# Kernel optimization log

Measured on AMD Instinct MI355X. Metric: run time of the kernel, lower is better.

The kernel has to match this reference:

```python
import math
import jax, jax.numpy as jnp
import numpy as np

THETA_BINS = 8
PHI_BINS = 8
BLOCK_SIZE = 15
MAX_PHI = math.pi
DVOL = 64  # input volume is DVOL^3
EPS = 2.220446049250313e-16  # sys.float_info.epsilon


def _sobel_weight():
    # Fixed (3,1,3,3,3) central-difference kernels: channel 0 = d/dz, 1 = d/dy, 2 = d/dx
    w = np.zeros((3, 1, 3, 3, 3), np.float32)
    w[0, 0, 0, 1, 1] = -1.0; w[0, 0, 2, 1, 1] = 1.0  # s_z
    w[1, 0, 1, 0, 1] = -1.0; w[1, 0, 1, 2, 1] = 1.0  # s_y
    w[2, 0, 1, 1, 0] = -1.0; w[2, 0, 1, 1, 2] = 1.0  # s_x
    return jnp.asarray(w)


def setup_inputs() -> dict:
    key = jax.random.key(0)
    x = jax.random.normal(key, (DVOL, DVOL, DVOL), dtype=jnp.float32)
    return {"x": x, "weight": _sobel_weight()}


def reference(x, weight):
    offset = BLOCK_SIZE // 2 + 1  # 8; output spatial = d + 2*offset - 2
    xb = x.astype(jnp.float32)[None, None]  # (1,1,d,h,w)
    out = jax.lax.conv_general_dilated(
        xb, weight, window_strides=(1, 1, 1),
        padding=[(offset, offset)] * 3,
        dimension_numbers=("NCDHW", "OIDHW", "NCDHW"))[0]  # (3, D, H, W)

    mag = jnp.sqrt(jnp.sum(out * out, axis=0))              # (D,H,W) frobenius over channel
    theta = jnp.arctan2(out[1], out[2])
    phi = jnp.arccos(out[0] / (mag + EPS))

    # NOTE: original code divides theta by max_phi_angle and scales by phi_bins (faithful)
    t_raw = theta / MAX_PHI * PHI_BINS
    p_raw = phi / MAX_PHI * PHI_BINS
    t_frac = t_raw - jnp.trunc(t_raw)  # torch.frac semantics
    p_frac = p_raw - jnp.trunc(p_raw)

    i0 = jnp.floor(t_raw).astype(jnp.int32) % THETA_BINS  # theta lower bin
    i1 = jnp.ceil(t_raw).astype(jnp.int32) % THETA_BINS   # theta upper bin
    i2 = jnp.floor(p_raw).astype(jnp.int32) % PHI_BINS    # phi lower bin
    i3 = jnp.ceil(p_raw).astype(jnp.int32) % PHI_BINS     # phi upper bin

    f0 = jnp.abs(t_frac); f1 = jnp.abs(1.0 - t_frac)
    f2 = jnp.abs(p_frac); f3 = jnp.abs(1.0 - p_frac)
    w0 = (f0 * f2) * mag  # scattered to (i0, i2) via scatter_ set
    w1 = (f0 * f3) * mag  # scatter_add at (i0, i3)
    w2 = (f1 * f2) * mag  # scatter_add at (i1, i2)

    # The torch scatter_/scatter_add_ chain (zero fill elsewhere, initial tensor zeros)
    # reduces exactly to three one-hot depositions per voxel; 4th add is absent
    # because the source forward is truncated after the third scatter_add_.
    tb = jnp.arange(THETA_BINS, dtype=jnp.int32)[:, None, None, None]  # (T,1,1,1)
    pb = jnp.arange(PHI_BINS, dtype=jnp.int32)[:, None, None, None]   # (P,1,1,1)
    t0 = (tb == i0).astype(mag.dtype)  # (T,D,H,W)
    t1 = (tb == i1).astype(mag.dtype)
    p2 = (pb == i2).astype(mag.dtype)  # (P,D,H,W)
    p3 = (pb == i3).astype(mag.dtype)

    out_plus_bins = (t0[:, None] * p2[None] * w0
                     + t0[:, None] * p3[None] * w1
                     + t1[:, None] * p2[None] * w2)  # (T,P,D,H,W)
    return out_plus_bins[None]  # (1, theta_bins, phi_bins, D, H, W)
```

## Files before the change

### kernel.cpp

```cpp
#include <hip/hip_runtime.h>
#include <math.h>


#define DVOL 64
#define S 78
#define S3 (S * S * S)
#define S3_4 (S3 / 4)

typedef float f32x4 __attribute__((ext_vector_type(4)));

__device__ __forceinline__ float ldx(const float* __restrict__ x, int z, int y, int xx) {
    if ((unsigned)z < (unsigned)DVOL && (unsigned)y < (unsigned)DVOL && (unsigned)xx < (unsigned)DVOL)
        return x[(z * DVOL + y) * DVOL + xx];
    return 0.0f;
}

__global__ void __launch_bounds__(256) hog_scatter4(const float* __restrict__ x,
                                                    f32x4* __restrict__ out) {
#pragma clang fp contract(off)
    int t4 = blockIdx.x * 256 + threadIdx.x;
    if (t4 >= S3_4) return;

    float wv0[4], wv1[4], wv2[4];
    int   b0[4],  b1[4],  b2[4];

    #pragma unroll
    for (int e = 0; e < 4; ++e) {
        int idx = t4 * 4 + e;
        int ox = idx % S;
        int r  = idx / S;
        int oy = r % S;
        int oz = r / S;
        int ix = ox - 7, iy = oy - 7, iz = oz - 7;

        float gz = ldx(x, iz + 1, iy, ix) - ldx(x, iz - 1, iy, ix);
        float gy = ldx(x, iz, iy + 1, ix) - ldx(x, iz, iy - 1, ix);
        float gx = ldx(x, iz, iy, ix + 1) - ldx(x, iz, iy, ix - 1);

        float mag2 = (gz * gz + gy * gy) + gx * gx;
        float mag  = sqrtf(mag2);

        wv0[e] = 0.0f; wv1[e] = 0.0f; wv2[e] = 0.0f;
        b0[e] = -1; b1[e] = -1; b2[e] = -1;

        if (mag != 0.0f) {
            float theta = (float)atan2((double)gy, (double)gx);
            const float EPS32 = 2.220446049250313e-16f;
            float denom = mag + EPS32;
            float ratio = gz / denom;
            float phi = (float)acos((double)ratio);

            const float PI32 = 3.14159274101257324f;
            float t_raw = theta / PI32 * 8.0f;
            float p_raw = phi   / PI32 * 8.0f;

            float t_frac = t_raw - truncf(t_raw);
            float p_frac = p_raw - truncf(p_raw);

            int i0 = ((int)floorf(t_raw)) & 7;
            int i1 = ((int)ceilf (t_raw)) & 7;
            int i2 = ((int)floorf(p_raw)) & 7;
            int i3 = ((int)ceilf (p_raw)) & 7;

            float f0 = fabsf(t_frac), f1 = fabsf(1.0f - t_frac);
            float f2 = fabsf(p_frac), f3 = fabsf(1.0f - p_frac);
            float w0 = (f0 * f2) * mag;
            float w1 = (f0 * f3) * mag;
            float w2 = (f1 * f2) * mag;

            int c0 = i0 * 8 + i2, c1 = i0 * 8 + i3, c2 = i1 * 8 + i2;
            if (c1 == c0) { w0 = w0 + w1; c1 = -1; }
            if (c2 == c0) { w0 = w0 + w2; c2 = -1; }

            wv0[e] = w0; wv1[e] = w1; wv2[e] = w2;
            b0[e]  = c0; b1[e]  = c1; b2[e]  = c2;
        }
    }

    #pragma unroll
    for (int p = 0; p < 64; ++p) {
        f32x4 o;
        #pragma unroll
        for (int e = 0; e < 4; ++e) {
            float v = 0.0f;
            if (p == b0[e]) v = wv0[e];
            if (p == b1[e]) v = wv1[e];
            if (p == b2[e]) v = wv2[e];
            o[e] = v;
        }
        __builtin_nontemporal_store(o, &out[(size_t)p * S3_4 + t4]);
    }
}

extern "C" void kernel_launch(void* const* d_in, const int* in_sizes, int n_in,
                              void* d_out, int out_size, void* d_ws, size_t ws_size,
                              hipStream_t stream) {
    const float* x = (const float*)d_in[0];
    f32x4* out = (f32x4*)d_out;

    const int threads = 256;
    const int blocks = (S3_4 + threads - 1) / threads;
    hog_scatter4<<<blocks, threads, 0, stream>>>(x, out);
}
```

Before: 140.3 us.

## Split HOG into angle-compute pass and parallel bin-group writer pass

The single kernel is split into two. The first pass computes the gradient, magnitude and raw theta/phi bin coordinates per voxel and writes them to workspace. The second pass launches 8x more blocks, each writing 8 of the 64 output bins, which spreads the heavy output stores across many more waves. Plain stores replace the nontemporal stores, and the single kernel is kept as a fallback when the workspace is too small. This adds an extra launch and workspace traffic in exchange for more store parallelism and less per-thread work.

```diff
diff --git a/kernel.cpp b/kernel.cpp
--- a/kernel.cpp
+++ b/kernel.cpp
@@ -6,6 +6,7 @@
 #define S 78
 #define S3 (S * S * S)
 #define S3_4 (S3 / 4)
+#define CHUNKS ((S3_4 + 255) / 256)
 
 typedef float f32x4 __attribute__((ext_vector_type(4)));
 
@@ -15,8 +16,99 @@
     return 0.0f;
 }
 
-__global__ void __launch_bounds__(256) hog_scatter4(const float* __restrict__ x,
-                                                    f32x4* __restrict__ out) {
+__global__ void __launch_bounds__(256) hog_pass1(const float* __restrict__ x,
+                                                 float* __restrict__ tr,
+                                                 float* __restrict__ pr,
+                                                 float* __restrict__ mg) {
+#pragma clang fp contract(off)
+    int idx = blockIdx.x * 256 + threadIdx.x;
+    if (idx >= S3) return;
+    int ox = idx % S;
+    int r  = idx / S;
+    int oy = r % S;
+    int oz = r / S;
+    int ix = ox - 7, iy = oy - 7, iz = oz - 7;
+
+    float gz = ldx(x, iz + 1, iy, ix) - ldx(x, iz - 1, iy, ix);
+    float gy = ldx(x, iz, iy + 1, ix) - ldx(x, iz, iy - 1, ix);
+    float gx = ldx(x, iz, iy, ix + 1) - ldx(x, iz, iy, ix - 1);
+
+    float mag2 = (gz * gz + gy * gy) + gx * gx;
+    float mag  = sqrtf(mag2);
+
+    float t_raw = 0.0f, p_raw = 0.0f;
+    if (mag != 0.0f) {
+        float theta = (float)atan2((double)gy, (double)gx);
+        const float EPS32 = 2.220446049250313e-16f;
+        float denom = mag + EPS32;
+        float ratio = gz / denom;
+        float phi = (float)acos((double)ratio);
+
+        const float PI32 = 3.14159274101257324f;
+        t_raw = theta / PI32 * 8.0f;
+        p_raw = phi   / PI32 * 8.0f;
+    }
+    tr[idx] = t_raw;
+    pr[idx] = p_raw;
+    mg[idx] = mag;
+}
+
+__global__ void __launch_bounds__(256) hog_pass2(const float* __restrict__ tr,
+                                                 const float* __restrict__ pr,
+                                                 const float* __restrict__ mg,
+                                                 f32x4* __restrict__ out) {
+#pragma clang fp contract(off)
+    int g = blockIdx.x / CHUNKS;
+    int c = blockIdx.x % CHUNKS;
+    int t4 = c * 256 + threadIdx.x;
+    if (t4 >= S3_4) return;
+
+    const f32x4 trv = reinterpret_cast<const f32x4*>(tr)[t4];
+    const f32x4 prv = reinterpret_cast<const f32x4*>(pr)[t4];
+    const f32x4 mgv = reinterpret_cast<const f32x4*>(mg)[t4];
+
+    f32x4 acc[8];
+    #pragma unroll
+    for (int p = 0; p < 8; ++p) acc[p] = (f32x4)(0.0f);
+
+    #pragma unroll
+    for (int e = 0; e < 4; ++e) {
+        float t_raw = trv[e], p_raw = prv[e], mag = mgv[e];
+
+        float t_frac = t_raw - truncf(t_raw);
+        float p_frac = p_raw - truncf(p_raw);
+
+        int i0 = ((int)floorf(t_raw)) & 7;
+        int i1 = ((int)ceilf (t_raw)) & 7;
+        int i2 = ((int)floorf(p_raw)) & 7;
+        int i3 = ((int)ceilf (p_raw)) & 7;
+
+        float f0 = fabsf(t_frac), f1 = fabsf(1.0f - t_frac);
+        float f2 = fabsf(p_frac), f3 = fabsf(1.0f - p_frac);
+        float w0 = (f0 * f2) * mag;
+        float w1 = (f0 * f3) * mag;
+        float w2 = (f1 * f2) * mag;
+
+        int b0 = i0 * 8 + i2, b1 = i0 * 8 + i3, b2 = i1 * 8 + i2;
+        if (b1 == b0) { w0 = w0 + w1; b1 = -1; }
+        if (b2 == b0) { w0 = w0 + w2; b2 = -1; }
+
+        #pragma unroll
+        for (int p = 0; p < 8; ++p) {
+            int bin = g * 8 + p;
+            float v = (bin == b0) ? w0 : ((bin == b1) ? w1 : ((bin == b2) ? w2 : 0.0f));
+            acc[p][e] = v;
+        }
+    }
+
+    #pragma unroll
+    for (int p = 0; p < 8; ++p) {
+        out[(size_t)(g * 8 + p) * S3_4 + t4] = acc[p];
+    }
+}
+
+__global__ void __launch_bounds__(256) hog_single(const float* __restrict__ x,
+                                                  f32x4* __restrict__ out) {
 #pragma clang fp contract(off)
     int t4 = blockIdx.x * 256 + threadIdx.x;
     if (t4 >= S3_4) return;
@@ -88,7 +180,7 @@
             if (p == b2[e]) v = wv2[e];
             o[e] = v;
         }
-        __builtin_nontemporal_store(o, &out[(size_t)p * S3_4 + t4]);
+        out[(size_t)p * S3_4 + t4] = o;
     }
 }
 
@@ -98,7 +190,14 @@
     const float* x = (const float*)d_in[0];
     f32x4* out = (f32x4*)d_out;
 
-    const int threads = 256;
-    const int blocks = (S3_4 + threads - 1) / threads;
-    hog_scatter4<<<blocks, threads, 0, stream>>>(x, out);
-}
+    const size_t need = (size_t)S3 * 3 * sizeof(float);
+    if (d_ws != nullptr && ws_size >= need) {
+        float* tr = (float*)d_ws;
+        float* pr = tr + S3;
+        float* mg = tr + 2 * (size_t)S3;
+        hog_pass1<<<(S3 + 255) / 256, 256, 0, stream>>>(x, tr, pr, mg);
+        hog_pass2<<<8 * CHUNKS, 256, 0, stream>>>(tr, pr, mg, out);
+    } else {
+        hog_single<<<CHUNKS, 256, 0, stream>>>(x, out);
+    }
+}
```

After: 130.6 us. 6.9% less time.
